# Kernel optimization log

Measured on AMD Instinct MI355X. Metric: run time of the kernel, lower is better.

## Reference

```python
import jax, jax.numpy as jnp
import numpy as np

# Mamba2Config-derived constants
N_LAYER = 4
D_MODEL = 1024
D_STATE = 128
D_CONV = 4
EXPAND = 2
HEADDIM = 64
CHUNK = 64
VOCAB = 50288  # 50277 padded to multiple of 16
D_INNER = EXPAND * D_MODEL          # 2048
NHEADS = D_INNER // HEADDIM          # 32
D_IN_PROJ = 2 * D_INNER + 2 * D_STATE + NHEADS  # 4384
CONV_DIM = D_INNER + 2 * D_STATE     # 2304
B, L = 1, 1024
EPS = 1e-5


def segsum(x):
    # x: (..., T) -> (..., T, T) stable segment-sum; exp() gives 1-semiseparable matrix
    T = x.shape[-1]
    xe = jnp.broadcast_to(x[..., :, None], x.shape + (T,))
    strict_lower = jnp.tril(jnp.ones((T, T), dtype=bool), -1)
    xe = jnp.where(strict_lower, xe, 0.0)
    s = jnp.cumsum(xe, axis=-2)
    lower = jnp.tril(jnp.ones((T, T), dtype=bool), 0)
    return jnp.where(lower, s, -jnp.inf)


def ssd(x, A, Bm, Cm, chunk):
    # x: (b,l,h,p), A: (b,l,h), Bm/Cm: (b,l,1,n)
    b, l, h, p = x.shape
    c = l // chunk
    x = x.reshape(b, c, chunk, h, p)
    A = A.reshape(b, c, chunk, h)
    Bm = Bm.reshape(b, c, chunk, 1, Bm.shape[-1])
    Cm = Cm.reshape(b, c, chunk, 1, Cm.shape[-1])
    A = jnp.transpose(A, (0, 3, 1, 2))           # (b,h,c,l)
    A_cs = jnp.cumsum(A, axis=-1)
    Lmat = jnp.exp(segsum(A))                    # (b,h,c,l,l)
    Y_diag = jnp.einsum('bclhn,bcshn,bhcls,bcshp->bclhp', Cm, Bm, Lmat, x)
    decay_states = jnp.exp(A_cs[:, :, :, -1:] - A_cs)
    states = jnp.einsum('bclhn,bhcl,bclhp->bchpn', Bm, decay_states, x)
    states = jnp.concatenate([jnp.zeros_like(states[:, :1]), states], axis=1)
    decay_chunk = jnp.exp(segsum(jnp.pad(A_cs[:, :, :, -1], ((0, 0), (0, 0), (1, 0)))))
    new_states = jnp.einsum('bhzc,bchpn->bzhpn', decay_chunk, states)
    Y_off = jnp.einsum('bclhn,bchpn,bhcl->bclhp', Cm, new_states[:, :-1], jnp.exp(A_cs))
    return (Y_diag + Y_off).reshape(b, l, h, p), new_states[:, -1]


def rmsnorm(x, w, z=None):
    if z is not None:
        x = x * (z * jax.nn.sigmoid(z))  # gated: x * silu(z)
    return x * jax.lax.rsqrt(jnp.mean(x * x, axis=-1, keepdims=True) + EPS) * w


def mamba2_block(u, in_w, conv_w, conv_b, dt_bias, A_log, D_p, gnorm_w, out_w):
    b, l, _ = u.shape
    A = -jnp.exp(A_log)                                      # (h,)
    zxbcdt = u @ in_w.T                                      # (b,l,D_IN_PROJ)
    z = zxbcdt[..., :D_INNER]
    xBC = zxbcdt[..., D_INNER:D_INNER + CONV_DIM]
    dt = zxbcdt[..., D_INNER + CONV_DIM:]
    dt = jax.nn.softplus(dt + dt_bias)                       # (b,l,h)
    # causal depthwise conv1d (kernel D_CONV) + silu
    xp = jnp.pad(xBC, ((0, 0), (D_CONV - 1, 0), (0, 0)))
    conv = jax.lax.conv_general_dilated(
        xp, conv_w[:, None, :], window_strides=(1,), padding='VALID',
        dimension_numbers=('NLC', 'OIL', 'NLC'), feature_group_count=CONV_DIM) + conv_b
    xBCs = conv * jax.nn.sigmoid(conv)
    x = xBCs[..., :D_INNER].reshape(b, l, NHEADS, HEADDIM)
    Bm = xBCs[..., D_INNER:D_INNER + D_STATE][:, :, None, :]
    Cm = xBCs[..., D_INNER + D_STATE:][:, :, None, :]
    y, _ = ssd(x * dt[..., None], A * dt, Bm, Cm, CHUNK)
    y = y + x * D_p[:, None]
    y = y.reshape(b, l, D_INNER)
    y = rmsnorm(y, gnorm_w, z=z)
    return y @ out_w.T


def setup_inputs() -> dict:
    key = jax.random.key(0)
    ks = jax.random.split(key, 12)
    inp = {
        'input_ids': jax.random.randint(ks[0], (B, L), 0, 50277, dtype=jnp.int32),
        'embedding': jax.random.normal(ks[1], (VOCAB, D_MODEL), jnp.float32) * 0.02,
        'norm_ws': jnp.ones((N_LAYER, D_MODEL), jnp.float32),
        'in_ws': jax.random.normal(ks[2], (N_LAYER, D_IN_PROJ, D_MODEL), jnp.float32) * 0.02,
        'conv_ws': jax.random.normal(ks[3], (N_LAYER, CONV_DIM, D_CONV), jnp.float32) * 0.2,
        'conv_bs': jnp.zeros((N_LAYER, CONV_DIM), jnp.float32),
        'dt_biases': jax.random.normal(ks[4], (N_LAYER, NHEADS), jnp.float32) * 0.5,
        'A_logs': jax.random.normal(ks[5], (N_LAYER, NHEADS), jnp.float32) * 0.5,
        'Ds': jnp.ones((N_LAYER, NHEADS), jnp.float32) + jax.random.normal(ks[6], (N_LAYER, NHEADS), jnp.float32) * 0.1,
        'gnorm_ws': jnp.ones((N_LAYER, D_INNER), jnp.float32),
        'out_ws': jax.random.normal(ks[7], (N_LAYER, D_MODEL, D_INNER), jnp.float32) * 0.02,
        'norm_f_w': jnp.ones((D_MODEL,), jnp.float32),
    }
    return inp


def reference(input_ids, embedding, norm_ws, in_ws, conv_ws, conv_bs, dt_biases,
              A_logs, Ds, gnorm_ws, out_ws, norm_f_w):
    x = embedding[input_ids]                     # (B,L,D_MODEL)
    for i in range(N_LAYER):
        x = x + mamba2_block(rmsnorm(x, norm_ws[i]), in_ws[i], conv_ws[i], conv_bs[i],
                             dt_biases[i], A_logs[i], Ds[i], gnorm_ws[i], out_ws[i])
    x = rmsnorm(x, norm_f_w)
    return x @ embedding.T                       # tied lm_head: (B,L,VOCAB)
```

## Files before the change

### kernel.cpp

```cpp
#include <hip/hip_runtime.h>
#include <math.h>

#define D_MODEL 1024
#define D_STATE 128
#define NHEADS 32
#define HEADDIM 64
#define D_INNER 2048
#define D_IN_PROJ 4384
#define CONV_DIM 2304
#define LSEQ 1024
#define NCHUNK 16
#define VOCAB 50288
#define EPSF 1e-5f

#define NPAD_INPROJ 4480
#define NPAD_VOCAB  50304

#define CP 132

typedef __bf16 bf16x8 __attribute__((ext_vector_type(8)));
typedef float  f32x4  __attribute__((ext_vector_type(4)));
typedef unsigned int u32;

__device__ __forceinline__ float silu_f(float v){ return v / (1.f + expf(-v)); }

__device__ __forceinline__ unsigned short f2bf(float f){
  unsigned int u = __float_as_uint(f);
  unsigned int r = (u + 0x7FFFu + ((u >> 16) & 1u)) >> 16;
  return (unsigned short)r;
}

__device__ __forceinline__ void gld_lds16(const void* g, void* l){
  __builtin_amdgcn_global_load_lds((const __attribute__((address_space(1))) u32*)g,
                                   (__attribute__((address_space(3))) u32*)l, 16, 0, 0);
}

__global__ __launch_bounds__(256) void castpad_k(const float* __restrict__ in,
                                                 unsigned short* __restrict__ out,
                                                 long n_in, long n_out){
  long i = ((long)blockIdx.x*256 + threadIdx.x)*8;
  if(i >= n_out) return;
  unsigned short v[8];
  if(i + 8 <= n_in){
    #pragma unroll
    for(int j=0;j<8;j++) v[j] = f2bf(in[i+j]);
  } else {
    #pragma unroll
    for(int j=0;j<8;j++){ long k=i+j; v[j] = (k < n_in) ? f2bf(in[k]) : (unsigned short)0; }
  }
  *(uint4*)&out[i] = *(const uint4*)v;
}

__global__ __launch_bounds__(256) void embed_k(const int* __restrict__ ids,
                                               const float* __restrict__ emb,
                                               float* __restrict__ x){
  int l = blockIdx.x;
  int d = blockIdx.y*256 + threadIdx.x;
  x[(size_t)l*D_MODEL + d] = emb[(size_t)ids[l]*D_MODEL + d];
}

__global__ __launch_bounds__(256) void rmsnorm_k(const float* __restrict__ x,
                                                 const float* __restrict__ w,
                                                 unsigned short* __restrict__ out, int D){
  int l = blockIdx.x;
  __shared__ float red[256];
  float s = 0.f;
  for(int i=threadIdx.x;i<D;i+=256){ float v = x[(size_t)l*D+i]; s += v*v; }
  red[threadIdx.x]=s; __syncthreads();
  for(int st=128;st>0;st>>=1){ if(threadIdx.x<st) red[threadIdx.x]+=red[threadIdx.x+st]; __syncthreads(); }
  float scale = rsqrtf(red[0]/(float)D + EPSF);
  for(int i=threadIdx.x;i<D;i+=256) out[(size_t)l*D+i] = f2bf(x[(size_t)l*D+i]*scale*w[i]);
}

__global__ __launch_bounds__(256) void gemm_bt_mfma(
  const unsigned short* __restrict__ A, const unsigned short* __restrict__ B,
  const float* __restrict__ res, float* __restrict__ C,
  int M, int Nc, int K)
{
  __shared__ unsigned short sA[2][128*32];
  __shared__ unsigned short sB[2][128*32];
  const int tid  = threadIdx.x;
  const int wave = tid >> 6, lane = tid & 63;

  const int nwg  = gridDim.x*gridDim.y;
  const int flat = blockIdx.x + gridDim.x*blockIdx.y;
  const int per  = nwg >> 3;
  const int w    = (flat & 7)*per + (flat >> 3);
  const int m0 = (w % gridDim.x)*128;
  const int n0 = (w / gridDim.x)*128;

  const int wm = wave >> 1, wn = wave & 1;
  const int llo = lane & 15, lhi = lane >> 4;

  const int eb0 = wave*1024;
  const int e0  = eb0 + lane*8;
  const int r0  = e0 >> 5, c0 = e0 & 31;
  const int eb1 = eb0 + 512;
  const int e1  = eb1 + lane*8;
  const int r1  = e1 >> 5, c1 = e1 & 31;

  f32x4 acc[4][4] = {};

  const int nt = K >> 5;
  gld_lds16(A + (size_t)(m0+r0)*K + c0, &sA[0][eb0]);
  gld_lds16(A + (size_t)(m0+r1)*K + c1, &sA[0][eb1]);
  gld_lds16(B + (size_t)(n0+r0)*K + c0, &sB[0][eb0]);
  gld_lds16(B + (size_t)(n0+r1)*K + c1, &sB[0][eb1]);
  __syncthreads();

  int cur = 0;
  for(int t=0;t<nt;t++){
    if(t+1 < nt){
      const int k0 = (t+1) << 5;
      gld_lds16(A + (size_t)(m0+r0)*K + k0 + c0, &sA[cur^1][eb0]);
      gld_lds16(A + (size_t)(m0+r1)*K + k0 + c1, &sA[cur^1][eb1]);
      gld_lds16(B + (size_t)(n0+r0)*K + k0 + c0, &sB[cur^1][eb0]);
      gld_lds16(B + (size_t)(n0+r1)*K + k0 + c1, &sB[cur^1][eb1]);
    }
    bf16x8 af[4], bfv[4];
    #pragma unroll
    for(int q=0;q<4;q++){
      af[q]  = *(const bf16x8*)&sA[cur][(wm*64 + q*16 + llo)*32 + lhi*8];
      bfv[q] = *(const bf16x8*)&sB[cur][(wn*64 + q*16 + llo)*32 + lhi*8];
    }
    #pragma unroll
    for(int i=0;i<4;i++)
      #pragma unroll
      for(int j=0;j<4;j++)
        acc[i][j] = __builtin_amdgcn_mfma_f32_16x16x32_bf16(af[i], bfv[j], acc[i][j], 0, 0, 0);
    __syncthreads();
    cur ^= 1;
  }

  #pragma unroll
  for(int i=0;i<4;i++){
    #pragma unroll
    for(int j=0;j<4;j++){
      const int n = n0 + wn*64 + j*16 + llo;
      if(n < Nc){
        #pragma unroll
        for(int r=0;r<4;r++){
          const int m = m0 + wm*64 + i*16 + lhi*4 + r;
          float v = acc[i][j][r];
          if(res) v += res[(size_t)m*Nc + n];
          C[(size_t)m*Nc + n] = v;
        }
      }
    }
  }
}

__global__ __launch_bounds__(256) void dt_k(const float* __restrict__ zxbcdt,
                                            const float* __restrict__ dt_bias,
                                            const float* __restrict__ A_log,
                                            float* __restrict__ dt, float* __restrict__ dA){
  int idx = blockIdx.x*256 + threadIdx.x;
  int l = idx >> 5, h = idx & 31;
  float v = zxbcdt[(size_t)l*D_IN_PROJ + D_INNER + CONV_DIM + h] + dt_bias[h];
  float sp = v > 20.f ? v : log1pf(expf(v));
  dt[idx] = sp;
  dA[idx] = -expf(A_log[h]) * sp;
}

__global__ __launch_bounds__(256) void conv_silu_k(const float* __restrict__ zxbcdt,
                                                   const float* __restrict__ cw,
                                                   const float* __restrict__ cb,
                                                   float* __restrict__ xBCs){
  int c = blockIdx.x*256 + threadIdx.x;
  int l = blockIdx.y;
  if(c >= CONV_DIM) return;
  float acc = cb[c];
  #pragma unroll
  for(int j=0;j<4;j++){
    int t = l - 3 + j;
    if(t >= 0) acc += zxbcdt[(size_t)t*D_IN_PROJ + D_INNER + c] * cw[c*4+j];
  }
  xBCs[(size_t)l*CONV_DIM + c] = silu_f(acc);
}

__global__ __launch_bounds__(256) void chunk_k(
  const float* __restrict__ xBCs, const float* __restrict__ dt, const float* __restrict__ dA,
  float* __restrict__ ydiag, float* __restrict__ states,
  float* __restrict__ acs_out, float* __restrict__ easum_out)
{
  const int c = blockIdx.x, h = blockIdx.y;
  __shared__ float sB[64][CP];
  __shared__ float sC[64][CP];
  __shared__ float sX[64][64];
  __shared__ float sM[64][64];
  __shared__ float sDec[64];
  __shared__ float acs[64];
  const int tid = threadIdx.x;
  for(int i=tid;i<2048;i+=256){
    int t=i>>5, n=(i&31)<<2; int l=c*64+t;
    float4 bv = *(const float4*)&xBCs[(size_t)l*CONV_DIM + D_INNER + n];
    float4 cv = *(const float4*)&xBCs[(size_t)l*CONV_DIM + D_INNER + D_STATE + n];
    *(float4*)&sB[t][n] = bv;
    *(float4*)&sC[t][n] = cv;
  }
  for(int i=tid;i<1024;i+=256){
    int t=i>>4, p=(i&15)<<2; int l=c*64+t;
    float4 xv = *(const float4*)&xBCs[(size_t)l*CONV_DIM + h*64 + p];
    float dtl = dt[l*32+h];
    xv.x*=dtl; xv.y*=dtl; xv.z*=dtl; xv.w*=dtl;
    *(float4*)&sX[t][p] = xv;
  }
  if(tid==0){ float s=0.f; for(int t=0;t<64;t++){ s+=dA[(c*64+t)*32+h]; acs[t]=s; } }
  __syncthreads();
  if(tid<64) sDec[tid]=expf(acs[63]-acs[tid]);
  for(int i=tid;i<4096;i+=256){
    int t=i>>6, s=i&63;
    float v=0.f;
    if(s<=t){
      const float4* c4=(const float4*)sC[t];
      const float4* b4=(const float4*)sB[s];
      float4 g={0,0,0,0};
      #pragma unroll 8
      for(int n=0;n<32;n++){ float4 cv=c4[n], bv=b4[n];
        g.x+=cv.x*bv.x; g.y+=cv.y*bv.y; g.z+=cv.z*bv.z; g.w+=cv.w*bv.w; }
      v=(g.x+g.y+g.z+g.w)*expf(acs[t]-acs[s]);
    }
    sM[t][s]=v;
  }
  __syncthreads();
  for(int i=tid;i<1024;i+=256){
    int t=i>>4, p4=(i&15)*4;
    float4 acc={0,0,0,0};
    for(int s=0;s<=t;s++){
      float m=sM[t][s];
      float4 xv=*(const float4*)&sX[s][p4];
      acc.x+=m*xv.x; acc.y+=m*xv.y; acc.z+=m*xv.z; acc.w+=m*xv.w;
    }
    int l=c*64+t;
    *(float4*)&ydiag[(size_t)l*D_INNER + h*64 + p4]=acc;
  }
  for(int i=tid;i<2048;i+=256){
    int p=i>>5, n4=(i&31)*4;
    float4 acc={0,0,0,0};
    for(int t=0;t<64;t++){
      float w=sX[t][p]*sDec[t];
      float4 bv=*(const float4*)&sB[t][n4];
      acc.x+=w*bv.x; acc.y+=w*bv.y; acc.z+=w*bv.z; acc.w+=w*bv.w;
    }
    *(float4*)&states[((size_t)(c*32+h)*64 + p)*128 + n4]=acc;
  }
  for(int t=tid;t<64;t+=256) acs_out[(c*32+h)*64+t]=acs[t];
  if(tid==0) easum_out[c*32+h]=expf(acs[63]);
}

__global__ __launch_bounds__(256) void scan_k(const float* __restrict__ states,
                                              const float* __restrict__ easum,
                                              float* __restrict__ istates){
  int idx = blockIdx.x*256 + threadIdx.x;
  int h = idx >> 13;
  float S = 0.f;
  for(int c=0;c<NCHUNK;c++){
    size_t off = (size_t)c*262144 + idx;
    istates[off] = S;
    S = S*easum[c*32+h] + states[off];
  }
}

__global__ __launch_bounds__(256) void yoff_k(
  const float* __restrict__ xBCs, const float* __restrict__ istates,
  const float* __restrict__ acs_in, const float* __restrict__ Ds,
  float* __restrict__ y)
{
  const int c=blockIdx.x, h=blockIdx.y;
  __shared__ float sS[64][CP];
  __shared__ float sC[64][CP];
  __shared__ float sE[64];
  const int tid=threadIdx.x;
  for(int i=tid;i<2048;i+=256){
    int t=i>>5, n=(i&31)<<2;
    float4 sv = *(const float4*)&istates[(size_t)c*262144 + h*8192 + (size_t)t*128 + n];
    float4 cv = *(const float4*)&xBCs[(size_t)(c*64+t)*CONV_DIM + D_INNER + D_STATE + n];
    *(float4*)&sS[t][n] = sv;
    *(float4*)&sC[t][n] = cv;
  }
  if(tid<64) sE[tid]=expf(acs_in[(c*32+h)*64+tid]);
  __syncthreads();
  const float Dh=Ds[h];
  for(int i=tid;i<4096;i+=256){
    int t=i>>6, p=i&63;
    const float4* c4=(const float4*)sC[t];
    const float4* s4=(const float4*)sS[p];
    float4 g={0,0,0,0};
    #pragma unroll 8
    for(int n=0;n<32;n++){ float4 cv=c4[n], sv=s4[n];
      g.x+=cv.x*sv.x; g.y+=cv.y*sv.y; g.z+=cv.z*sv.z; g.w+=cv.w*sv.w; }
    int l=c*64+t;
    size_t yi=(size_t)l*D_INNER + h*64 + p;
    float xorig=xBCs[(size_t)l*CONV_DIM + h*64 + p];
    y[yi] = y[yi] + sE[t]*(g.x+g.y+g.z+g.w) + xorig*Dh;
  }
}

__global__ __launch_bounds__(256) void gnorm_k(const float* __restrict__ y,
                                               const float* __restrict__ zxbcdt,
                                               const float* __restrict__ w,
                                               unsigned short* __restrict__ out){
  int l=blockIdx.x;
  __shared__ float red[256];
  float s=0.f;
  for(int i=threadIdx.x;i<D_INNER;i+=256){
    float z=zxbcdt[(size_t)l*D_IN_PROJ + i];
    float v=y[(size_t)l*D_INNER+i]*silu_f(z);
    s+=v*v;
  }
  red[threadIdx.x]=s; __syncthreads();
  for(int st=128;st>0;st>>=1){ if(threadIdx.x<st) red[threadIdx.x]+=red[threadIdx.x+st]; __syncthreads(); }
  float scale=rsqrtf(red[0]/(float)D_INNER + EPSF);
  for(int i=threadIdx.x;i<D_INNER;i+=256){
    float z=zxbcdt[(size_t)l*D_IN_PROJ + i];
    float v=y[(size_t)l*D_INNER+i]*silu_f(z);
    out[(size_t)l*D_INNER+i]=f2bf(v*scale*w[i]);
  }
}

extern "C" void kernel_launch(void* const* d_in, const int* in_sizes, int n_in,
                              void* d_out, int out_size, void* d_ws, size_t ws_size,
                              hipStream_t stream)
{
  const int*   ids      = (const int*)  d_in[0];
  const float* emb      = (const float*)d_in[1];
  const float* norm_ws  = (const float*)d_in[2];
  const float* in_ws    = (const float*)d_in[3];
  const float* conv_ws  = (const float*)d_in[4];
  const float* conv_bs  = (const float*)d_in[5];
  const float* dt_bias  = (const float*)d_in[6];
  const float* A_logs   = (const float*)d_in[7];
  const float* Ds       = (const float*)d_in[8];
  const float* gnorm_ws = (const float*)d_in[9];
  const float* out_ws   = (const float*)d_in[10];
  const float* norm_f_w = (const float*)d_in[11];
  float* out = (float*)d_out;

  float* ws      = (float*)d_ws;
  float* x       = ws;
  float* zxbcdt  = x + 1048576;
  float* xBCs    = zxbcdt + 4489216;
  float* dtb     = xBCs + 2359296;
  float* dAb     = dtb + 32768;
  float* acs     = dAb + 32768;
  float* easum   = acs + 32768;
  float* yb      = easum + 512;
  float* states  = yb + 2097152;
  float* istates = states + 4194304;
  unsigned short* bfbase   = (unsigned short*)(istates + 4194304);
  unsigned short* u_bf     = bfbase;
  unsigned short* yg_bf    = u_bf  + 1048576;
  unsigned short* in_wb    = yg_bf + 2097152;
  unsigned short* out_wb   = in_wb + 4587520;
  unsigned short* emb_bf   = out_wb + 2097152;

  embed_k<<<dim3(1024,4),256,0,stream>>>(ids, emb, x);
  castpad_k<<<25152,256,0,stream>>>(emb, emb_bf, (long)VOCAB*D_MODEL, (long)NPAD_VOCAB*D_MODEL);

  for(int i=0;i<4;i++){
    rmsnorm_k<<<1024,256,0,stream>>>(x, norm_ws + i*1024, u_bf, D_MODEL);
    castpad_k<<<2240,256,0,stream>>>(in_ws + (size_t)i*4489216, in_wb,
                                     4489216L, (long)NPAD_INPROJ*D_MODEL);
    gemm_bt_mfma<<<dim3(8,35),256,0,stream>>>(u_bf, in_wb, nullptr, zxbcdt,
                                              1024, D_IN_PROJ, D_MODEL);
    dt_k<<<128,256,0,stream>>>(zxbcdt, dt_bias + i*32, A_logs + i*32, dtb, dAb);
    conv_silu_k<<<dim3(9,1024),256,0,stream>>>(zxbcdt, conv_ws + i*(CONV_DIM*4),
                                               conv_bs + i*CONV_DIM, xBCs);
    chunk_k<<<dim3(16,32),256,0,stream>>>(xBCs, dtb, dAb, yb, states, acs, easum);
    scan_k<<<1024,256,0,stream>>>(states, easum, istates);
    yoff_k<<<dim3(16,32),256,0,stream>>>(xBCs, istates, acs, Ds + i*32, yb);
    gnorm_k<<<1024,256,0,stream>>>(yb, zxbcdt, gnorm_ws + i*D_INNER, yg_bf);
    castpad_k<<<1024,256,0,stream>>>(out_ws + (size_t)i*2097152, out_wb, 2097152L, 2097152L);
    gemm_bt_mfma<<<dim3(8,8),256,0,stream>>>(yg_bf, out_wb, x, x,
                                             1024, D_MODEL, D_INNER);
  }

  rmsnorm_k<<<1024,256,0,stream>>>(x, norm_f_w, u_bf, D_MODEL);
  gemm_bt_mfma<<<dim3(8,393),256,0,stream>>>(u_bf, emb_bf, nullptr, out,
                                             1024, VOCAB, D_MODEL);
}
```

Before: 1.358 ms.

## Widen GEMM K-tile with swizzled LDS and hoist head-independent C·B Gram matrix

The GEMM now stages 64-wide K tiles into a larger LDS buffer with an XOR swizzle, swaps the MFMA operand order, and writes results as float4 along N. The aim is fewer loop iterations and barriers, fewer LDS bank conflicts, and wider stores. Separately, the C·Bᵀ Gram matrix does not depend on the head, so it is computed once per chunk in a new kernel instead of 32 times. The chunk kernel then only applies the decay mask, and its cumulative sum becomes a wave-shuffle scan. The trade-off is an extra launch, a global round-trip for the Gram matrix, and more LDS per GEMM block, which may lower occupancy.

After: 1.277 ms. 6.0% less time.

```diff
diff --git a/kernel.cpp b/kernel.cpp
--- a/kernel.cpp
+++ b/kernel.cpp
@@ -77,8 +77,8 @@
   const float* __restrict__ res, float* __restrict__ C,
   int M, int Nc, int K)
 {
-  __shared__ unsigned short sA[2][128*32];
-  __shared__ unsigned short sB[2][128*32];
+  __shared__ unsigned short sA[2][128*64];
+  __shared__ unsigned short sB[2][128*64];
   const int tid  = threadIdx.x;
   const int wave = tid >> 6, lane = tid & 63;
 
@@ -92,59 +92,64 @@
   const int wm = wave >> 1, wn = wave & 1;
   const int llo = lane & 15, lhi = lane >> 4;
 
-  const int eb0 = wave*1024;
-  const int e0  = eb0 + lane*8;
-  const int r0  = e0 >> 5, c0 = e0 & 31;
-  const int eb1 = eb0 + 512;
-  const int e1  = eb1 + lane*8;
-  const int r1  = e1 >> 5, c1 = e1 & 31;
+  const int scol = (((lane&7) ^ (lane>>3)) << 3);
+  int srow[4];
+  #pragma unroll
+  for(int q=0;q<4;q++) srow[q] = q*32 + wave*8 + (lane>>3);
+  const int sbase0 = wave*512;
 
   f32x4 acc[4][4] = {};
-
-  const int nt = K >> 5;
-  gld_lds16(A + (size_t)(m0+r0)*K + c0, &sA[0][eb0]);
-  gld_lds16(A + (size_t)(m0+r1)*K + c1, &sA[0][eb1]);
-  gld_lds16(B + (size_t)(n0+r0)*K + c0, &sB[0][eb0]);
-  gld_lds16(B + (size_t)(n0+r1)*K + c1, &sB[0][eb1]);
+  const int nt = K >> 6;
+
+  #pragma unroll
+  for(int q=0;q<4;q++){
+    gld_lds16(A + (size_t)(m0+srow[q])*K + scol, &sA[0][q*2048 + sbase0]);
+    gld_lds16(B + (size_t)(n0+srow[q])*K + scol, &sB[0][q*2048 + sbase0]);
+  }
   __syncthreads();
 
   int cur = 0;
   for(int t=0;t<nt;t++){
     if(t+1 < nt){
-      const int k0 = (t+1) << 5;
-      gld_lds16(A + (size_t)(m0+r0)*K + k0 + c0, &sA[cur^1][eb0]);
-      gld_lds16(A + (size_t)(m0+r1)*K + k0 + c1, &sA[cur^1][eb1]);
-      gld_lds16(B + (size_t)(n0+r0)*K + k0 + c0, &sB[cur^1][eb0]);
-      gld_lds16(B + (size_t)(n0+r1)*K + k0 + c1, &sB[cur^1][eb1]);
-    }
-    bf16x8 af[4], bfv[4];
+      const int k0 = (t+1) << 6;
+      #pragma unroll
+      for(int q=0;q<4;q++){
+        gld_lds16(A + (size_t)(m0+srow[q])*K + k0 + scol, &sA[cur^1][q*2048 + sbase0]);
+        gld_lds16(B + (size_t)(n0+srow[q])*K + k0 + scol, &sB[cur^1][q*2048 + sbase0]);
+      }
+    }
     #pragma unroll
-    for(int q=0;q<4;q++){
-      af[q]  = *(const bf16x8*)&sA[cur][(wm*64 + q*16 + llo)*32 + lhi*8];
-      bfv[q] = *(const bf16x8*)&sB[cur][(wn*64 + q*16 + llo)*32 + lhi*8];
-    }
-    #pragma unroll
-    for(int i=0;i<4;i++)
+    for(int kk=0;kk<2;kk++){
+      bf16x8 af[4], bfv[4];
+      const int ck = (((lhi + kk*4) ^ (llo&7)) << 3);
       #pragma unroll
-      for(int j=0;j<4;j++)
-        acc[i][j] = __builtin_amdgcn_mfma_f32_16x16x32_bf16(af[i], bfv[j], acc[i][j], 0, 0, 0);
+      for(int q=0;q<4;q++){
+        af[q]  = *(const bf16x8*)&sA[cur][(wm*64 + q*16 + llo)*64 + ck];
+        bfv[q] = *(const bf16x8*)&sB[cur][(wn*64 + q*16 + llo)*64 + ck];
+      }
+      #pragma unroll
+      for(int i=0;i<4;i++)
+        #pragma unroll
+        for(int j=0;j<4;j++)
+          acc[i][j] = __builtin_amdgcn_mfma_f32_16x16x32_bf16(bfv[j], af[i], acc[i][j], 0, 0, 0);
+    }
     __syncthreads();
     cur ^= 1;
   }
 
   #pragma unroll
   for(int i=0;i<4;i++){
+    const int m = m0 + wm*64 + i*16 + llo;
     #pragma unroll
     for(int j=0;j<4;j++){
-      const int n = n0 + wn*64 + j*16 + llo;
-      if(n < Nc){
-        #pragma unroll
-        for(int r=0;r<4;r++){
-          const int m = m0 + wm*64 + i*16 + lhi*4 + r;
-          float v = acc[i][j][r];
-          if(res) v += res[(size_t)m*Nc + n];
-          C[(size_t)m*Nc + n] = v;
+      const int nb = n0 + wn*64 + j*16 + lhi*4;
+      if(nb < Nc){
+        float4 v = *(float4*)&acc[i][j];
+        if(res){
+          float4 rv = *(const float4*)&res[(size_t)m*Nc + nb];
+          v.x+=rv.x; v.y+=rv.y; v.z+=rv.z; v.w+=rv.w;
         }
+        *(float4*)&C[(size_t)m*Nc + nb] = v;
       }
     }
   }
@@ -178,36 +183,18 @@
   xBCs[(size_t)l*CONV_DIM + c] = silu_f(acc);
 }
 
-__global__ __launch_bounds__(256) void chunk_k(
-  const float* __restrict__ xBCs, const float* __restrict__ dt, const float* __restrict__ dA,
-  float* __restrict__ ydiag, float* __restrict__ states,
-  float* __restrict__ acs_out, float* __restrict__ easum_out)
-{
-  const int c = blockIdx.x, h = blockIdx.y;
+__global__ __launch_bounds__(256) void gcb_k(const float* __restrict__ xBCs,
+                                             float* __restrict__ gbuf){
+  const int c = blockIdx.x;
   __shared__ float sB[64][CP];
   __shared__ float sC[64][CP];
-  __shared__ float sX[64][64];
-  __shared__ float sM[64][64];
-  __shared__ float sDec[64];
-  __shared__ float acs[64];
   const int tid = threadIdx.x;
   for(int i=tid;i<2048;i+=256){
     int t=i>>5, n=(i&31)<<2; int l=c*64+t;
-    float4 bv = *(const float4*)&xBCs[(size_t)l*CONV_DIM + D_INNER + n];
-    float4 cv = *(const float4*)&xBCs[(size_t)l*CONV_DIM + D_INNER + D_STATE + n];
-    *(float4*)&sB[t][n] = bv;
-    *(float4*)&sC[t][n] = cv;
-  }
-  for(int i=tid;i<1024;i+=256){
-    int t=i>>4, p=(i&15)<<2; int l=c*64+t;
-    float4 xv = *(const float4*)&xBCs[(size_t)l*CONV_DIM + h*64 + p];
-    float dtl = dt[l*32+h];
-    xv.x*=dtl; xv.y*=dtl; xv.z*=dtl; xv.w*=dtl;
-    *(float4*)&sX[t][p] = xv;
-  }
-  if(tid==0){ float s=0.f; for(int t=0;t<64;t++){ s+=dA[(c*64+t)*32+h]; acs[t]=s; } }
+    *(float4*)&sB[t][n] = *(const float4*)&xBCs[(size_t)l*CONV_DIM + D_INNER + n];
+    *(float4*)&sC[t][n] = *(const float4*)&xBCs[(size_t)l*CONV_DIM + D_INNER + D_STATE + n];
+  }
   __syncthreads();
-  if(tid<64) sDec[tid]=expf(acs[63]-acs[tid]);
   for(int i=tid;i<4096;i+=256){
     int t=i>>6, s=i&63;
     float v=0.f;
@@ -218,9 +205,55 @@
       #pragma unroll 8
       for(int n=0;n<32;n++){ float4 cv=c4[n], bv=b4[n];
         g.x+=cv.x*bv.x; g.y+=cv.y*bv.y; g.z+=cv.z*bv.z; g.w+=cv.w*bv.w; }
-      v=(g.x+g.y+g.z+g.w)*expf(acs[t]-acs[s]);
-    }
-    sM[t][s]=v;
+      v=g.x+g.y+g.z+g.w;
+    }
+    gbuf[(size_t)c*4096 + i]=v;
+  }
+}
+
+__global__ __launch_bounds__(256) void chunk_k(
+  const float* __restrict__ xBCs, const float* __restrict__ dt, const float* __restrict__ dA,
+  const float* __restrict__ gbuf,
+  float* __restrict__ ydiag, float* __restrict__ states,
+  float* __restrict__ acs_out, float* __restrict__ easum_out)
+{
+  const int c = blockIdx.x, h = blockIdx.y;
+  __shared__ float sB[64][CP];
+  __shared__ float sM[64][64];
+  __shared__ float sX[64][64];
+  __shared__ float sDec[64];
+  __shared__ float acs[64];
+  const int tid = threadIdx.x;
+  const int wave = tid>>6, lane = tid&63;
+
+  for(int i=tid;i<2048;i+=256){
+    int t=i>>5, n=(i&31)<<2; int l=c*64+t;
+    *(float4*)&sB[t][n] = *(const float4*)&xBCs[(size_t)l*CONV_DIM + D_INNER + n];
+  }
+  for(int i=tid;i<1024;i+=256){
+    int t=i>>4, p=(i&15)<<2; int l=c*64+t;
+    float4 xv = *(const float4*)&xBCs[(size_t)l*CONV_DIM + h*64 + p];
+    float dtl = dt[l*32+h];
+    xv.x*=dtl; xv.y*=dtl; xv.z*=dtl; xv.w*=dtl;
+    *(float4*)&sX[t][p] = xv;
+  }
+  for(int i=tid;i<4096;i+=256) ((float*)sM)[i] = gbuf[(size_t)c*4096 + i];
+  if(wave==0){
+    float a = dA[(size_t)(c*64+lane)*32 + h];
+    #pragma unroll
+    for(int off=1;off<64;off<<=1){
+      float up = __shfl_up(a, off, 64);
+      if(lane>=off) a += up;
+    }
+    acs[lane]=a;
+    float tot = __shfl(a, 63, 64);
+    sDec[lane]=expf(tot-a);
+    if(lane==63) easum_out[c*32+h]=expf(a);
+  }
+  __syncthreads();
+  for(int i=tid;i<4096;i+=256){
+    int t=i>>6, s=i&63;
+    sM[t][s] = (s<=t) ? sM[t][s]*expf(acs[t]-acs[s]) : 0.f;
   }
   __syncthreads();
   for(int i=tid;i<1024;i+=256){
@@ -245,7 +278,6 @@
     *(float4*)&states[((size_t)(c*32+h)*64 + p)*128 + n4]=acc;
   }
   for(int t=tid;t<64;t+=256) acs_out[(c*32+h)*64+t]=acs[t];
-  if(tid==0) easum_out[c*32+h]=expf(acs[63]);
 }
 
 __global__ __launch_bounds__(256) void scan_k(const float* __restrict__ states,
@@ -344,7 +376,8 @@
   float* dAb     = dtb + 32768;
   float* acs     = dAb + 32768;
   float* easum   = acs + 32768;
-  float* yb      = easum + 512;
+  float* gbuf    = easum + 512;
+  float* yb      = gbuf + 65536;
   float* states  = yb + 2097152;
   float* istates = states + 4194304;
   unsigned short* bfbase   = (unsigned short*)(istates + 4194304);
@@ -366,7 +399,8 @@
     dt_k<<<128,256,0,stream>>>(zxbcdt, dt_bias + i*32, A_logs + i*32, dtb, dAb);
     conv_silu_k<<<dim3(9,1024),256,0,stream>>>(zxbcdt, conv_ws + i*(CONV_DIM*4),
                                                conv_bs + i*CONV_DIM, xBCs);
-    chunk_k<<<dim3(16,32),256,0,stream>>>(xBCs, dtb, dAb, yb, states, acs, easum);
+    gcb_k<<<16,256,0,stream>>>(xBCs, gbuf);
+    chunk_k<<<dim3(16,32),256,0,stream>>>(xBCs, dtb, dAb, gbuf, yb, states, acs, easum);
     scan_k<<<1024,256,0,stream>>>(states, easum, istates);
     yoff_k<<<dim3(16,32),256,0,stream>>>(xBCs, istates, acs, Ds + i*32, yb);
     gnorm_k<<<1024,256,0,stream>>>(yb, zxbcdt, gnorm_ws + i*D_INNER, yg_bf);
```
